# Performance work log

Measured on AMD Instinct MI355X. Metric: run time of the kernel, lower is better.

Reference implementation:

```python
import jax, jax.numpy as jnp
import numpy as np

B = 256      # graphs per batch
N = 512      # nodes per graph
FEAT = 64    # num_features
H = 64       # nhid
DEG = 16     # avg degree
RATIO = 0.5  # pooling_ratio
E = B * N * DEG


def setup_inputs() -> dict:
    key = jax.random.key(0)
    ks = jax.random.split(key, 12)
    # edges constructed within each graph via offsets
    src_loc = jax.random.randint(ks[0], (B, N * DEG), 0, N)
    dst_loc = jax.random.randint(ks[1], (B, N * DEG), 0, N)
    offs = (jnp.arange(B) * N)[:, None]
    edge_src = (src_loc + offs).reshape(-1).astype(jnp.int32)
    edge_dst = (dst_loc + offs).reshape(-1).astype(jnp.int32)
    batch = jnp.repeat(jnp.arange(B, dtype=jnp.int32), N)
    x = jax.random.normal(ks[2], (B * N, FEAT), dtype=jnp.float32)
    edge_attr = jax.random.uniform(ks[3], (E,), dtype=jnp.float32) + 0.1
    s1 = 1.0 / np.sqrt(FEAT)
    s2 = 1.0 / np.sqrt(H)
    return {
        "x": x,
        "edge_attr": edge_attr,
        "W1": jax.random.normal(ks[4], (FEAT, H), jnp.float32) * s1,
        "b1": jnp.zeros((H,), jnp.float32),
        "Wp1": jax.random.normal(ks[5], (H, 1), jnp.float32) * s2,
        "bp1": jnp.zeros((1,), jnp.float32),
        "W2": jax.random.normal(ks[6], (H, H), jnp.float32) * s2,
        "b2": jnp.zeros((H,), jnp.float32),
        "Wp2": jax.random.normal(ks[7], (H, 1), jnp.float32) * s2,
        "bp2": jnp.zeros((1,), jnp.float32),
        "edge_src": edge_src,
        "edge_dst": edge_dst,
        "batch": batch,
    }


def gcn_conv(x, W, b, src, dst, ew, n):
    """PyG GCNConv: sym-normalized weighted adjacency + self-loops (weight 1)."""
    h = x @ W                                   # [n, out]
    deg = jnp.zeros((n,), x.dtype).at[dst].add(ew) + 1.0  # self-loop adds 1
    dinv = jax.lax.rsqrt(deg)
    coef = dinv[dst] * ew * dinv[src]           # [E]
    out = jnp.zeros_like(h).at[dst].add(coef[:, None] * h[src])
    out = out + h * (1.0 / deg)[:, None]        # self-loop term: deg^-0.5 * 1 * deg^-0.5
    return out + b


def sag_pool(x, src, dst, ew, Wp, bp, n_per):
    """SAGPool: score = GCNConv(x)->1, per-graph top-k, gate by tanh(score),
    filter edges (dropped edges represented by zero weight)."""
    n = x.shape[0]
    score = gcn_conv(x, Wp, bp, src, dst, ew, n)[:, 0]   # [n]
    k = int(np.ceil(RATIO * n_per))
    _, idx = jax.lax.top_k(score.reshape(B, n_per), k)   # [B, k] local indices
    perm = (idx + (jnp.arange(B) * n_per)[:, None]).reshape(-1)
    xn = x[perm] * jnp.tanh(score[perm])[:, None]        # [B*k, H]
    newid = jnp.full((n,), -1, jnp.int32).at[perm].set(
        jnp.arange(B * k, dtype=jnp.int32))
    ns, nd = newid[src], newid[dst]
    valid = (ns >= 0) & (nd >= 0)
    ew2 = jnp.where(valid, ew, 0.0)
    ns = jnp.where(valid, ns, 0)
    nd = jnp.where(valid, nd, 0)
    return xn, ns, nd, ew2, k


def readout(x, k):
    """[gmp || gap] per graph; each graph has exactly k nodes, contiguous."""
    xg = x.reshape(B, k, -1)
    return jnp.concatenate([xg.max(axis=1), xg.mean(axis=1)], axis=1)  # [B, 2H]


def reference(x, edge_attr, W1, b1, Wp1, bp1, W2, b2, Wp2, bp2,
              edge_src, edge_dst, batch):
    n0 = x.shape[0]
    h = jax.nn.relu(gcn_conv(x, W1, b1, edge_src, edge_dst, edge_attr, n0))
    h, s1, d1, w1e, k1 = sag_pool(h, edge_src, edge_dst, edge_attr, Wp1, bp1, N)
    x1 = readout(h, k1)
    h = jax.nn.relu(gcn_conv(h, W2, b2, s1, d1, w1e, B * k1))
    h, _, _, _, k2 = sag_pool(h, s1, d1, w1e, Wp2, bp2, k1)
    x2 = readout(h, k2)
    return (x1 + x2) / 2.0
```

## Files before the change

kernel.cpp:

```cpp
#include <hip/hip_runtime.h>
#include <math.h>

#define BG   256
#define NN   512
#define EPG  (NN * 16)
#define NE   (BG * EPG)
#define N0   (BG * NN)
#define K1   256
#define N1_  (BG * K1)
#define K2   128
#define N2_  (BG * K2)

__device__ __forceinline__ float4 f4fma(float s, float4 a, float4 c) {
    c.x = fmaf(s, a.x, c.x); c.y = fmaf(s, a.y, c.y);
    c.z = fmaf(s, a.z, c.z); c.w = fmaf(s, a.w, c.w);
    return c;
}

template <int NPG, bool REMAP>
__global__ __launch_bounds__(512)
void stage_head_kernel(const int* __restrict__ esrc, const int* __restrict__ edst,
                       const float* __restrict__ eatt, const int* __restrict__ nid,
                       int2* __restrict__ pairs, int* __restrict__ rowstart,
                       int* __restrict__ rowcnt, float* __restrict__ dinv,
                       const float4* __restrict__ X4, const float4* __restrict__ W4,
                       float4* __restrict__ Y4, int nrows, int mmb) {
    __shared__ __align__(16) char smem[52224];
    if ((int)blockIdx.x < BG) {
        int2*  lpair = (int2*)smem;
        int*   cnt   = (int*)(smem + 32768);
        float* wsum  = (float*)(smem + 32768) + NPG;
        int*   scn   = (int*)(smem + 32768) + 2 * NPG;
        float* sdinv = (float*)(smem + 32768) + 3 * NPG;
        int*   wtot  = (int*)(smem + 32768) + 4 * NPG;
        int g = blockIdx.x;
        int e0 = g * EPG, nbase = g * NPG;
        for (int ii = threadIdx.x; ii < NPG; ii += 512) { cnt[ii] = 0; wsum[ii] = 0.f; }
        __syncthreads();
        const int4*   edst4 = (const int4*)(edst + e0);
        const int4*   esrc4 = (const int4*)(esrc + e0);
        const float4* eatt4 = (const float4*)(eatt + e0);
        int ed[16]; int es[16]; float ea[16];
#pragma unroll
        for (int c = 0; c < 4; ++c) {
            int ch = threadIdx.x + c * 512;
            int4   dd = edst4[ch];
            int4   ss = esrc4[ch];
            float4 ww = eatt4[ch];
            ed[c * 4 + 0] = dd.x; ed[c * 4 + 1] = dd.y; ed[c * 4 + 2] = dd.z; ed[c * 4 + 3] = dd.w;
            es[c * 4 + 0] = ss.x; es[c * 4 + 1] = ss.y; es[c * 4 + 2] = ss.z; es[c * 4 + 3] = ss.w;
            ea[c * 4 + 0] = ww.x; ea[c * 4 + 1] = ww.y; ea[c * 4 + 2] = ww.z; ea[c * 4 + 3] = ww.w;
        }
        if (REMAP) {
#pragma unroll
            for (int j = 0; j < 16; ++j) { ed[j] = nid[ed[j]]; es[j] = nid[es[j]]; }
        }
#pragma unroll
        for (int j = 0; j < 16; ++j) {
            bool valid = !REMAP || (ed[j] >= 0 && es[j] >= 0);
            if (valid) {
                int dl = ed[j] - nbase;
                atomicAdd(&cnt[dl], 1);
                atomicAdd(&wsum[dl], ea[j]);
            }
        }
        __syncthreads();
        int i = threadIdx.x;
        int lane = i & 63, wvid = i >> 6;
        int xval = (i < NPG) ? cnt[i] : 0;
        int xs = xval;
#pragma unroll
        for (int off = 1; off < 64; off <<= 1) {
            int v = __shfl_up(xs, off, 64);
            if (lane >= off) xs += v;
        }
        if (lane == 63) wtot[wvid] = xs;
        __syncthreads();
        int woff = 0, total = 0;
#pragma unroll
        for (int t = 0; t < 8; ++t) {
            int wt = wtot[t];
            if (t < wvid) woff += wt;
            total += wt;
        }
        xs += woff;
        if (i < NPG) {
            int st = xs - xval;
            rowstart[nbase + i] = e0 + st;
            rowcnt[nbase + i]   = xval;
            float di = rsqrtf(wsum[i] + 1.0f);
            dinv[nbase + i] = di;
            sdinv[i] = di;
            scn[i] = st;
        }
        __syncthreads();
        int slots[16]; float cf[16];
#pragma unroll
        for (int j = 0; j < 16; ++j) {
            bool valid = !REMAP || (ed[j] >= 0 && es[j] >= 0);
            slots[j] = -1;
            if (valid) {
                int dl = ed[j] - nbase, sl = es[j] - nbase;
                cf[j] = sdinv[dl] * ea[j] * sdinv[sl];
                slots[j] = atomicAdd(&scn[dl], 1);
            }
        }
#pragma unroll
        for (int j = 0; j < 16; ++j)
            if (slots[j] >= 0 && slots[j] < 4096)
                lpair[slots[j]] = make_int2(es[j] - nbase, __float_as_int(cf[j]));
        __syncthreads();
        int n0 = total < 4096 ? total : 4096;
        for (int k = threadIdx.x; k < n0; k += 512) pairs[e0 + k] = lpair[k];
        __syncthreads();
        if (total > 4096) {
#pragma unroll
            for (int j = 0; j < 16; ++j)
                if (slots[j] >= 4096)
                    lpair[slots[j] - 4096] = make_int2(es[j] - nbase, __float_as_int(cf[j]));
            __syncthreads();
            int n1 = total - 4096;
            for (int k = threadIdx.x; k < n1; k += 512) pairs[e0 + 4096 + k] = lpair[k];
        }
    } else {
        float (*sW)[68] = (float (*)[68])smem;
        int p = threadIdx.x >> 8;
        int t = threadIdx.x & 255;
        float (*sX)[68] = (float (*)[68])(smem + 17408 + p * 17408);
#pragma unroll
        for (int u = 0; u < 2; ++u) {
            int idx = threadIdx.x + u * 512;
            int r = idx >> 4, c4 = idx & 15;
            *(float4*)&sW[r][c4 * 4] = W4[idx];
        }
        int mb = blockIdx.x - BG;
        int ntiles = nrows >> 6;
        int rg = t >> 4, cg = t & 15;
        for (int tile = mb * 2 + p; tile < ntiles; tile += mmb * 2) {
            __syncthreads();
            int row0 = tile << 6;
#pragma unroll
            for (int u = 0; u < 4; ++u) {
                int idx = t + u * 256;
                int r = idx >> 4, c4 = idx & 15;
                *(float4*)&sX[r][c4 * 4] = X4[(size_t)(row0 + r) * 16 + c4];
            }
            __syncthreads();
            float4 acc0 = make_float4(0.f, 0.f, 0.f, 0.f);
            float4 acc1 = acc0, acc2 = acc0, acc3 = acc0;
#pragma unroll
            for (int k4 = 0; k4 < 16; ++k4) {
                float4 xv0 = *(const float4*)&sX[rg * 4 + 0][k4 * 4];
                float4 xv1 = *(const float4*)&sX[rg * 4 + 1][k4 * 4];
                float4 xv2 = *(const float4*)&sX[rg * 4 + 2][k4 * 4];
                float4 xv3 = *(const float4*)&sX[rg * 4 + 3][k4 * 4];
                float4 wv0 = *(const float4*)&sW[k4 * 4 + 0][cg * 4];
                float4 wv1 = *(const float4*)&sW[k4 * 4 + 1][cg * 4];
                float4 wv2 = *(const float4*)&sW[k4 * 4 + 2][cg * 4];
                float4 wv3 = *(const float4*)&sW[k4 * 4 + 3][cg * 4];
                acc0 = f4fma(xv0.x, wv0, acc0); acc0 = f4fma(xv0.y, wv1, acc0);
                acc0 = f4fma(xv0.z, wv2, acc0); acc0 = f4fma(xv0.w, wv3, acc0);
                acc1 = f4fma(xv1.x, wv0, acc1); acc1 = f4fma(xv1.y, wv1, acc1);
                acc1 = f4fma(xv1.z, wv2, acc1); acc1 = f4fma(xv1.w, wv3, acc1);
                acc2 = f4fma(xv2.x, wv0, acc2); acc2 = f4fma(xv2.y, wv1, acc2);
                acc2 = f4fma(xv2.z, wv2, acc2); acc2 = f4fma(xv2.w, wv3, acc2);
                acc3 = f4fma(xv3.x, wv0, acc3); acc3 = f4fma(xv3.y, wv1, acc3);
                acc3 = f4fma(xv3.z, wv2, acc3); acc3 = f4fma(xv3.w, wv3, acc3);
            }
            size_t ob = (size_t)(row0 + rg * 4) * 16 + cg;
            Y4[ob]      = acc0;
            Y4[ob + 16] = acc1;
            Y4[ob + 32] = acc2;
            Y4[ob + 48] = acc3;
        }
    }
}

template <int NPG, int K, bool FINAL>
__global__ __launch_bounds__(1024)
void tail_kernel(const float4* __restrict__ hx4, const int2* __restrict__ pairs,
                 const int* __restrict__ rowstart, const int* __restrict__ rowcnt,
                 const float* __restrict__ dinv, const float4* __restrict__ b4,
                 const float4* __restrict__ wp4, const float* __restrict__ bp,
                 int* __restrict__ nid, float4* __restrict__ xn4,
                 float* __restrict__ xr, const float* __restrict__ x1r,
                 float* __restrict__ out) {
    constexpr int PASSES = NPG / 32;
    constexpr int LPN = 1024 / NPG;
    constexpr int LOG_LPN = (LPN == 2) ? 1 : 2;
    constexpr int QF = 16 / LPN;
    constexpr int RLOG = (NPG == 512) ? 9 : 8;
    constexpr int RCH = NPG * NPG / 1024;
    constexpr int SH_A  = NPG * 68;
    constexpr int SH_UN = 4096;
    __shared__ __align__(16) float smem[SH_A + SH_UN + 2 * NPG + 64 + 64];
    float*  shx  = smem;
    int*    perm = (int*)(smem + SH_A);
    float*  shp  = smem + SH_A + NPG;
    float4* smx  = (float4*)(smem + SH_A);
    float4* ssm  = (float4*)(smem + SH_A + 2048);
    float*  ssc  = smem + SH_A + SH_UN;
    int*    rnk  = (int*)(smem + SH_A + SH_UN + NPG);
    float*  sbw  = smem + SH_A + SH_UN + 2 * NPG;
    int*    hist = (int*)(smem + SH_A + SH_UN + 2 * NPG + 64);

    int g = blockIdx.x, nbase = g * NPG;
    int t = threadIdx.x;
    int lane16 = t & 15, lane = t & 63;

    for (int i = t; i < NPG * 16; i += 1024) {
        int r = i >> 4, c4 = i & 15;
        *(float4*)&shx[r * 68 + c4 * 4] = hx4[(size_t)nbase * 16 + i];
    }
    if (t < 64) { sbw[t] = ((const float*)b4)[t]; hist[t] = 0; }
    for (int i = t; i < NPG; i += 1024) rnk[i] = 0;
    __syncthreads();
    for (int i = t; i < NPG; i += 1024) {
        int c = min(rowcnt[nbase + i], 63);
        atomicAdd(&hist[c], 1);
    }
    __syncthreads();
    if (t < 64) {
        int v = hist[t], s = v;
#pragma unroll
        for (int off = 1; off < 64; off <<= 1) {
            int u = __shfl_up(s, off, 64);
            if (lane >= off) s += u;
        }
        hist[t] = s - v;
    }
    __syncthreads();
    for (int i = t; i < NPG; i += 1024) {
        int c = min(rowcnt[nbase + i], 63);
        int pos = atomicAdd(&hist[c], 1);
        perm[pos] = i;
    }
    __syncthreads();
    {
        int idx2 = t >> LOG_LPN;
        int half = t & (LPN - 1);
        int nl = perm[idx2];
        int st = rowstart[nbase + nl], cn = rowcnt[nbase + nl];
        float di = dinv[nbase + nl], dii = di * di;
        int fb = half * QF;
        float4 acc[QF];
#pragma unroll
        for (int c = 0; c < QF; ++c) {
            float4 xv = *(const float4*)&shx[nl * 68 + (fb + c) * 4];
            acc[c].x = fmaf(xv.x, dii, sbw[(fb + c) * 4 + 0]);
            acc[c].y = fmaf(xv.y, dii, sbw[(fb + c) * 4 + 1]);
            acc[c].z = fmaf(xv.z, dii, sbw[(fb + c) * 4 + 2]);
            acc[c].w = fmaf(xv.w, dii, sbw[(fb + c) * 4 + 3]);
        }
        int2 p0 = (cn > 0) ? pairs[st] : make_int2(0, 0);
        int2 p1 = (cn > 1) ? pairs[st + 1] : make_int2(0, 0);
        for (int j = 0; j < cn; ++j) {
            int2 p2 = (j + 2 < cn) ? pairs[st + j + 2] : make_int2(0, 0);
            float cf = __int_as_float(p0.y);
            int   s  = p0.x;
#pragma unroll
            for (int c = 0; c < QF; ++c)
                acc[c] = f4fma(cf, *(const float4*)&shx[s * 68 + (fb + c) * 4], acc[c]);
            p0 = p1; p1 = p2;
        }
#pragma unroll
        for (int c = 0; c < QF; ++c) {
            acc[c].x = fmaxf(acc[c].x, 0.f); acc[c].y = fmaxf(acc[c].y, 0.f);
            acc[c].z = fmaxf(acc[c].z, 0.f); acc[c].w = fmaxf(acc[c].w, 0.f);
        }
        __syncthreads();
#pragma unroll
        for (int c = 0; c < QF; ++c)
            *(float4*)&shx[nl * 68 + (fb + c) * 4] = acc[c];
    }
    __syncthreads();
    if (t < 512) {
        int wv8 = t >> 6, sub4 = (t >> 4) & 3;
        float4 w4 = wp4[lane16];
#pragma unroll
        for (int p = 0; p < PASSES; ++p) {
            int n2 = p * 32 + wv8 * 4 + sub4;
            float4 a = *(const float4*)&shx[n2 * 68 + lane16 * 4];
            float tt = a.x * w4.x + a.y * w4.y + a.z * w4.z + a.w * w4.w;
            tt += __shfl_xor(tt, 1, 64); tt += __shfl_xor(tt, 2, 64);
            tt += __shfl_xor(tt, 4, 64); tt += __shfl_xor(tt, 8, 64);
            if (lane16 == 0) shp[n2] = tt;
        }
    }
    __syncthreads();
    if (t < NPG) {
        int i = perm[t];
        int st = rowstart[nbase + i], cn = rowcnt[nbase + i];
        float di = dinv[nbase + i];
        float a = fmaf(shp[i], di * di, bp[0]);
        int2 q0 = (cn > 0) ? pairs[st] : make_int2(0, 0);
        int2 q1 = (cn > 1) ? pairs[st + 1] : make_int2(0, 0);
        for (int j = 0; j < cn; ++j) {
            int2 q2 = (j + 2 < cn) ? pairs[st + j + 2] : make_int2(0, 0);
            a = fmaf(__int_as_float(q0.y), shp[q0.x], a);
            q0 = q1; q1 = q2;
        }
        ssc[i] = a;
    }
    __syncthreads();
    {
        int part = t >> RLOG;
        int i = t & (NPG - 1);
        float si = ssc[i];
        int j0 = part * RCH;
        int rank = 0;
        for (int j = j0; j < j0 + RCH; j += 4) {
            float4 sj = *(const float4*)&ssc[j];
            rank += (sj.x > si) || (sj.x == si && j     < i);
            rank += (sj.y > si) || (sj.y == si && j + 1 < i);
            rank += (sj.z > si) || (sj.z == si && j + 2 < i);
            rank += (sj.w > si) || (sj.w == si && j + 3 < i);
        }
        atomicAdd(&rnk[i], rank);
    }
    __syncthreads();
    if (!FINAL)
        for (int i = t; i < NPG; i += 1024)
            nid[nbase + i] = (rnk[i] < K) ? (g * K + rnk[i]) : -1;
    float4 mx = make_float4(-3.402823466e38f, -3.402823466e38f, -3.402823466e38f, -3.402823466e38f);
    float4 sm = make_float4(0.f, 0.f, 0.f, 0.f);
    if (t < 512) {
        int wv8 = t >> 6, sub4 = (t >> 4) & 3;
#pragma unroll
        for (int p = 0; p < PASSES; ++p) {
            int n2 = p * 32 + wv8 * 4 + sub4;
            int r = rnk[n2];
            if (r < K) {
                float gt = tanhf(ssc[n2]);
                float4 v = *(const float4*)&shx[n2 * 68 + lane16 * 4];
                v.x *= gt; v.y *= gt; v.z *= gt; v.w *= gt;
                if (!FINAL) xn4[((size_t)g * K + r) * 16 + lane16] = v;
                mx.x = fmaxf(mx.x, v.x); mx.y = fmaxf(mx.y, v.y);
                mx.z = fmaxf(mx.z, v.z); mx.w = fmaxf(mx.w, v.w);
                sm.x += v.x; sm.y += v.y; sm.z += v.z; sm.w += v.w;
            }
        }
    }
    int grp = t >> 4;
    __syncthreads();
    if (t < 512) {
        smx[grp * 16 + lane16] = mx;
        ssm[grp * 16 + lane16] = sm;
    }
    __syncthreads();
    if (grp == 0) {
#pragma unroll
        for (int u = 1; u < 32; ++u) {
            float4 a = smx[u * 16 + lane16], b = ssm[u * 16 + lane16];
            mx.x = fmaxf(mx.x, a.x); mx.y = fmaxf(mx.y, a.y);
            mx.z = fmaxf(mx.z, a.z); mx.w = fmaxf(mx.w, a.w);
            sm.x += b.x; sm.y += b.y; sm.z += b.z; sm.w += b.w;
        }
        float invK = 1.f / K;
        int c = lane16 * 4;
        float mr[4] = {mx.x, mx.y, mx.z, mx.w};
        float ar[4] = {sm.x * invK, sm.y * invK, sm.z * invK, sm.w * invK};
#pragma unroll
        for (int u = 0; u < 4; ++u) {
            if (FINAL) {
                out[g * 128 + c + u]      = 0.5f * (x1r[g * 128 + c + u]      + mr[u]);
                out[g * 128 + 64 + c + u] = 0.5f * (x1r[g * 128 + 64 + c + u] + ar[u]);
            } else {
                xr[g * 128 + c + u]      = mr[u];
                xr[g * 128 + 64 + c + u] = ar[u];
            }
        }
    }
}

extern "C" void kernel_launch(void* const* d_in, const int* in_sizes, int n_in,
                              void* d_out, int out_size, void* d_ws, size_t ws_size,
                              hipStream_t stream) {
    const float* x    = (const float*)d_in[0];
    const float* eatt = (const float*)d_in[1];
    const float* W1   = (const float*)d_in[2];
    const float* b1   = (const float*)d_in[3];
    const float* Wp1  = (const float*)d_in[4];
    const float* bp1  = (const float*)d_in[5];
    const float* W2   = (const float*)d_in[6];
    const float* b2   = (const float*)d_in[7];
    const float* Wp2  = (const float*)d_in[8];
    const float* bp2  = (const float*)d_in[9];
    const int*   esrc = (const int*)d_in[10];
    const int*   edst = (const int*)d_in[11];
    float* out = (float*)d_out;

    float* ws = (float*)d_ws;
    size_t o = 0;
    float* A    = ws + o; o += (size_t)N0 * 64;
    float* xn1  = ws + o; o += (size_t)N1_ * 64;
    int2*  prs  = (int2*)(ws + o); o += (size_t)NE * 2;
    int*   rst  = (int*)(ws + o); o += N0;
    int*   rcn  = (int*)(ws + o); o += N0;
    float* dinv = ws + o; o += N0;
    int*   nid  = (int*)(ws + o); o += N0;
    float* x1r  = ws + o; o += BG * 128;

    float* hx1 = A;
    float* hx2 = A;

    stage_head_kernel<NN, false><<<BG + 512, 512, 0, stream>>>(
        esrc, edst, eatt, nullptr, prs, rst, rcn, dinv,
        (const float4*)x, (const float4*)W1, (float4*)hx1, N0, 512);
    tail_kernel<NN, K1, false><<<BG, 1024, 0, stream>>>(
        (const float4*)hx1, prs, rst, rcn, dinv, (const float4*)b1,
        (const float4*)Wp1, bp1, nid, (float4*)xn1, x1r, nullptr, nullptr);
    stage_head_kernel<K1, true><<<BG + 256, 512, 0, stream>>>(
        esrc, edst, eatt, nid, prs, rst, rcn, dinv,
        (const float4*)xn1, (const float4*)W2, (float4*)hx2, N1_, 256);
    tail_kernel<K1, K2, true><<<BG, 1024, 0, stream>>>(
        (const float4*)hx2, prs, rst, rcn, dinv, (const float4*)b2,
        (const float4*)Wp2, bp2, nullptr, nullptr, nullptr, x1r, out);
}
```

Baseline: 218.1 us.

## Fuse CSR build, feature matmul and tail into one per-graph stage kernel

Merges the head kernel (edge bucketing into CSR plus a separate matmul block range) with the tail kernel into a single per-graph kernel of 1024 threads. The matmul now runs from the node features already staged in shared memory and writes the result back into that buffer, so the intermediate feature matrix no longer round-trips through global memory and two launches are removed. The cost is that each stage now launches only 256 blocks, one per graph, so the matmul and edge work are serialized inside each block instead of overlapping across extra blocks, and register pressure rises from holding the accumulated tiles.

```diff
diff --git a/kernel.cpp b/kernel.cpp
--- a/kernel.cpp
+++ b/kernel.cpp
@@ -17,174 +17,18 @@
     return c;
 }
 
-template <int NPG, bool REMAP>
-__global__ __launch_bounds__(512)
-void stage_head_kernel(const int* __restrict__ esrc, const int* __restrict__ edst,
-                       const float* __restrict__ eatt, const int* __restrict__ nid,
-                       int2* __restrict__ pairs, int* __restrict__ rowstart,
-                       int* __restrict__ rowcnt, float* __restrict__ dinv,
-                       const float4* __restrict__ X4, const float4* __restrict__ W4,
-                       float4* __restrict__ Y4, int nrows, int mmb) {
-    __shared__ __align__(16) char smem[52224];
-    if ((int)blockIdx.x < BG) {
-        int2*  lpair = (int2*)smem;
-        int*   cnt   = (int*)(smem + 32768);
-        float* wsum  = (float*)(smem + 32768) + NPG;
-        int*   scn   = (int*)(smem + 32768) + 2 * NPG;
-        float* sdinv = (float*)(smem + 32768) + 3 * NPG;
-        int*   wtot  = (int*)(smem + 32768) + 4 * NPG;
-        int g = blockIdx.x;
-        int e0 = g * EPG, nbase = g * NPG;
-        for (int ii = threadIdx.x; ii < NPG; ii += 512) { cnt[ii] = 0; wsum[ii] = 0.f; }
-        __syncthreads();
-        const int4*   edst4 = (const int4*)(edst + e0);
-        const int4*   esrc4 = (const int4*)(esrc + e0);
-        const float4* eatt4 = (const float4*)(eatt + e0);
-        int ed[16]; int es[16]; float ea[16];
-#pragma unroll
-        for (int c = 0; c < 4; ++c) {
-            int ch = threadIdx.x + c * 512;
-            int4   dd = edst4[ch];
-            int4   ss = esrc4[ch];
-            float4 ww = eatt4[ch];
-            ed[c * 4 + 0] = dd.x; ed[c * 4 + 1] = dd.y; ed[c * 4 + 2] = dd.z; ed[c * 4 + 3] = dd.w;
-            es[c * 4 + 0] = ss.x; es[c * 4 + 1] = ss.y; es[c * 4 + 2] = ss.z; es[c * 4 + 3] = ss.w;
-            ea[c * 4 + 0] = ww.x; ea[c * 4 + 1] = ww.y; ea[c * 4 + 2] = ww.z; ea[c * 4 + 3] = ww.w;
-        }
-        if (REMAP) {
-#pragma unroll
-            for (int j = 0; j < 16; ++j) { ed[j] = nid[ed[j]]; es[j] = nid[es[j]]; }
-        }
-#pragma unroll
-        for (int j = 0; j < 16; ++j) {
-            bool valid = !REMAP || (ed[j] >= 0 && es[j] >= 0);
-            if (valid) {
-                int dl = ed[j] - nbase;
-                atomicAdd(&cnt[dl], 1);
-                atomicAdd(&wsum[dl], ea[j]);
-            }
-        }
-        __syncthreads();
-        int i = threadIdx.x;
-        int lane = i & 63, wvid = i >> 6;
-        int xval = (i < NPG) ? cnt[i] : 0;
-        int xs = xval;
-#pragma unroll
-        for (int off = 1; off < 64; off <<= 1) {
-            int v = __shfl_up(xs, off, 64);
-            if (lane >= off) xs += v;
-        }
-        if (lane == 63) wtot[wvid] = xs;
-        __syncthreads();
-        int woff = 0, total = 0;
-#pragma unroll
-        for (int t = 0; t < 8; ++t) {
-            int wt = wtot[t];
-            if (t < wvid) woff += wt;
-            total += wt;
-        }
-        xs += woff;
-        if (i < NPG) {
-            int st = xs - xval;
-            rowstart[nbase + i] = e0 + st;
-            rowcnt[nbase + i]   = xval;
-            float di = rsqrtf(wsum[i] + 1.0f);
-            dinv[nbase + i] = di;
-            sdinv[i] = di;
-            scn[i] = st;
-        }
-        __syncthreads();
-        int slots[16]; float cf[16];
-#pragma unroll
-        for (int j = 0; j < 16; ++j) {
-            bool valid = !REMAP || (ed[j] >= 0 && es[j] >= 0);
-            slots[j] = -1;
-            if (valid) {
-                int dl = ed[j] - nbase, sl = es[j] - nbase;
-                cf[j] = sdinv[dl] * ea[j] * sdinv[sl];
-                slots[j] = atomicAdd(&scn[dl], 1);
-            }
-        }
-#pragma unroll
-        for (int j = 0; j < 16; ++j)
-            if (slots[j] >= 0 && slots[j] < 4096)
-                lpair[slots[j]] = make_int2(es[j] - nbase, __float_as_int(cf[j]));
-        __syncthreads();
-        int n0 = total < 4096 ? total : 4096;
-        for (int k = threadIdx.x; k < n0; k += 512) pairs[e0 + k] = lpair[k];
-        __syncthreads();
-        if (total > 4096) {
-#pragma unroll
-            for (int j = 0; j < 16; ++j)
-                if (slots[j] >= 4096)
-                    lpair[slots[j] - 4096] = make_int2(es[j] - nbase, __float_as_int(cf[j]));
-            __syncthreads();
-            int n1 = total - 4096;
-            for (int k = threadIdx.x; k < n1; k += 512) pairs[e0 + 4096 + k] = lpair[k];
-        }
-    } else {
-        float (*sW)[68] = (float (*)[68])smem;
-        int p = threadIdx.x >> 8;
-        int t = threadIdx.x & 255;
-        float (*sX)[68] = (float (*)[68])(smem + 17408 + p * 17408);
-#pragma unroll
-        for (int u = 0; u < 2; ++u) {
-            int idx = threadIdx.x + u * 512;
-            int r = idx >> 4, c4 = idx & 15;
-            *(float4*)&sW[r][c4 * 4] = W4[idx];
-        }
-        int mb = blockIdx.x - BG;
-        int ntiles = nrows >> 6;
-        int rg = t >> 4, cg = t & 15;
-        for (int tile = mb * 2 + p; tile < ntiles; tile += mmb * 2) {
-            __syncthreads();
-            int row0 = tile << 6;
-#pragma unroll
-            for (int u = 0; u < 4; ++u) {
-                int idx = t + u * 256;
-                int r = idx >> 4, c4 = idx & 15;
-                *(float4*)&sX[r][c4 * 4] = X4[(size_t)(row0 + r) * 16 + c4];
-            }
-            __syncthreads();
-            float4 acc0 = make_float4(0.f, 0.f, 0.f, 0.f);
-            float4 acc1 = acc0, acc2 = acc0, acc3 = acc0;
-#pragma unroll
-            for (int k4 = 0; k4 < 16; ++k4) {
-                float4 xv0 = *(const float4*)&sX[rg * 4 + 0][k4 * 4];
-                float4 xv1 = *(const float4*)&sX[rg * 4 + 1][k4 * 4];
-                float4 xv2 = *(const float4*)&sX[rg * 4 + 2][k4 * 4];
-                float4 xv3 = *(const float4*)&sX[rg * 4 + 3][k4 * 4];
-                float4 wv0 = *(const float4*)&sW[k4 * 4 + 0][cg * 4];
-                float4 wv1 = *(const float4*)&sW[k4 * 4 + 1][cg * 4];
-                float4 wv2 = *(const float4*)&sW[k4 * 4 + 2][cg * 4];
-                float4 wv3 = *(const float4*)&sW[k4 * 4 + 3][cg * 4];
-                acc0 = f4fma(xv0.x, wv0, acc0); acc0 = f4fma(xv0.y, wv1, acc0);
-                acc0 = f4fma(xv0.z, wv2, acc0); acc0 = f4fma(xv0.w, wv3, acc0);
-                acc1 = f4fma(xv1.x, wv0, acc1); acc1 = f4fma(xv1.y, wv1, acc1);
-                acc1 = f4fma(xv1.z, wv2, acc1); acc1 = f4fma(xv1.w, wv3, acc1);
-                acc2 = f4fma(xv2.x, wv0, acc2); acc2 = f4fma(xv2.y, wv1, acc2);
-                acc2 = f4fma(xv2.z, wv2, acc2); acc2 = f4fma(xv2.w, wv3, acc2);
-                acc3 = f4fma(xv3.x, wv0, acc3); acc3 = f4fma(xv3.y, wv1, acc3);
-                acc3 = f4fma(xv3.z, wv2, acc3); acc3 = f4fma(xv3.w, wv3, acc3);
-            }
-            size_t ob = (size_t)(row0 + rg * 4) * 16 + cg;
-            Y4[ob]      = acc0;
-            Y4[ob + 16] = acc1;
-            Y4[ob + 32] = acc2;
-            Y4[ob + 48] = acc3;
-        }
-    }
-}
-
-template <int NPG, int K, bool FINAL>
+template <int NPG, int K, bool REMAP, bool FINAL>
 __global__ __launch_bounds__(1024)
-void tail_kernel(const float4* __restrict__ hx4, const int2* __restrict__ pairs,
-                 const int* __restrict__ rowstart, const int* __restrict__ rowcnt,
-                 const float* __restrict__ dinv, const float4* __restrict__ b4,
-                 const float4* __restrict__ wp4, const float* __restrict__ bp,
-                 int* __restrict__ nid, float4* __restrict__ xn4,
-                 float* __restrict__ xr, const float* __restrict__ x1r,
-                 float* __restrict__ out) {
+void stage_kernel(const int* __restrict__ esrc, const int* __restrict__ edst,
+                  const float* __restrict__ eatt, const int* __restrict__ nid_in,
+                  int* __restrict__ nid_out,
+                  int2* __restrict__ pairs, int* __restrict__ rowstart,
+                  int* __restrict__ rowcnt, float* __restrict__ dinv,
+                  const float4* __restrict__ X4, const float4* __restrict__ W4,
+                  const float4* __restrict__ b4, const float4* __restrict__ wp4,
+                  const float* __restrict__ bp,
+                  float4* __restrict__ xn4, float* __restrict__ xr,
+                  const float* __restrict__ x1r, float* __restrict__ out) {
     constexpr int PASSES = NPG / 32;
     constexpr int LPN = 1024 / NPG;
     constexpr int LOG_LPN = (LPN == 2) ? 1 : 2;
@@ -203,18 +47,164 @@
     int*    rnk  = (int*)(smem + SH_A + SH_UN + NPG);
     float*  sbw  = smem + SH_A + SH_UN + 2 * NPG;
     int*    hist = (int*)(smem + SH_A + SH_UN + 2 * NPG + 64);
-
-    int g = blockIdx.x, nbase = g * NPG;
+    int2*   lpair = (int2*)smem;
+    int*    cnt   = (int*)smem + 8192;
+    float*  wsum  = smem + 8192 + NPG;
+    int*    scn   = (int*)smem + 8192 + 2 * NPG;
+    float*  sdinv = smem + 8192 + 3 * NPG;
+    int*    wtot  = (int*)smem + 8192 + 4 * NPG;
+    float*  sWf   = smem + SH_A;
+
+    int g = blockIdx.x, nbase = g * NPG, e0 = g * EPG;
     int t = threadIdx.x;
     int lane16 = t & 15, lane = t & 63;
 
+    for (int i = t; i < NPG; i += 1024) { cnt[i] = 0; wsum[i] = 0.f; }
+    __syncthreads();
+    {
+        const int4*   edst4 = (const int4*)(edst + e0);
+        const int4*   esrc4 = (const int4*)(esrc + e0);
+        const float4* eatt4 = (const float4*)(eatt + e0);
+        int ed[8]; int es[8]; float ea[8];
+#pragma unroll
+        for (int c = 0; c < 2; ++c) {
+            int ch = t + c * 1024;
+            int4   dd = edst4[ch];
+            int4   ss = esrc4[ch];
+            float4 ww = eatt4[ch];
+            ed[c * 4 + 0] = dd.x; ed[c * 4 + 1] = dd.y; ed[c * 4 + 2] = dd.z; ed[c * 4 + 3] = dd.w;
+            es[c * 4 + 0] = ss.x; es[c * 4 + 1] = ss.y; es[c * 4 + 2] = ss.z; es[c * 4 + 3] = ss.w;
+            ea[c * 4 + 0] = ww.x; ea[c * 4 + 1] = ww.y; ea[c * 4 + 2] = ww.z; ea[c * 4 + 3] = ww.w;
+        }
+        if (REMAP) {
+#pragma unroll
+            for (int j = 0; j < 8; ++j) { ed[j] = nid_in[ed[j]]; es[j] = nid_in[es[j]]; }
+        }
+#pragma unroll
+        for (int j = 0; j < 8; ++j) {
+            bool valid = !REMAP || (ed[j] >= 0 && es[j] >= 0);
+            if (valid) {
+                int dl = ed[j] - nbase;
+                atomicAdd(&cnt[dl], 1);
+                atomicAdd(&wsum[dl], ea[j]);
+            }
+        }
+        __syncthreads();
+        int wv = t >> 6;
+        int xval = (t < NPG) ? cnt[t] : 0;
+        int xs = xval;
+#pragma unroll
+        for (int off = 1; off < 64; off <<= 1) {
+            int v = __shfl_up(xs, off, 64);
+            if (lane >= off) xs += v;
+        }
+        if (lane == 63) wtot[wv] = xs;
+        __syncthreads();
+        int woff = 0, total = 0;
+#pragma unroll
+        for (int w = 0; w < 16; ++w) {
+            int wt = wtot[w];
+            if (w < wv) woff += wt;
+            total += wt;
+        }
+        xs += woff;
+        if (t < NPG) {
+            int st = xs - xval;
+            rowstart[nbase + t] = e0 + st;
+            rowcnt[nbase + t]   = xval;
+            float di = rsqrtf(wsum[t] + 1.0f);
+            dinv[nbase + t] = di;
+            sdinv[t] = di;
+            scn[t] = st;
+        }
+        __syncthreads();
+        int slots[8]; float cf[8];
+#pragma unroll
+        for (int j = 0; j < 8; ++j) {
+            bool valid = !REMAP || (ed[j] >= 0 && es[j] >= 0);
+            slots[j] = -1;
+            if (valid) {
+                int dl = ed[j] - nbase, sl = es[j] - nbase;
+                cf[j] = sdinv[dl] * ea[j] * sdinv[sl];
+                slots[j] = atomicAdd(&scn[dl], 1);
+            }
+        }
+#pragma unroll
+        for (int j = 0; j < 8; ++j)
+            if (slots[j] >= 0 && slots[j] < 4096)
+                lpair[slots[j]] = make_int2(es[j] - nbase, __float_as_int(cf[j]));
+        __syncthreads();
+        int n0 = total < 4096 ? total : 4096;
+        for (int k2 = t; k2 < n0; k2 += 1024) pairs[e0 + k2] = lpair[k2];
+        __syncthreads();
+        if (total > 4096) {
+#pragma unroll
+            for (int j = 0; j < 8; ++j)
+                if (slots[j] >= 4096)
+                    lpair[slots[j] - 4096] = make_int2(es[j] - nbase, __float_as_int(cf[j]));
+            __syncthreads();
+            int n1 = total - 4096;
+            for (int k2 = t; k2 < n1; k2 += 1024) pairs[e0 + 4096 + k2] = lpair[k2];
+            __syncthreads();
+        }
+    }
+    __syncthreads();
+
     for (int i = t; i < NPG * 16; i += 1024) {
         int r = i >> 4, c4 = i & 15;
-        *(float4*)&shx[r * 68 + c4 * 4] = hx4[(size_t)nbase * 16 + i];
+        *(float4*)&shx[r * 68 + c4 * 4] = X4[(size_t)nbase * 16 + i];
+    }
+    {
+        int r = t >> 4, c4 = t & 15;
+        *(float4*)&sWf[r * 68 + c4 * 4] = W4[t];
+    }
+    __syncthreads();
+
+    {
+        constexpr int TILES = NPG / 64, TPG = TILES / 4;
+        int q = t >> 8, tq = t & 255;
+        int rg = tq >> 4, cg = tq & 15;
+        float4 ac[TPG][4];
+#pragma unroll
+        for (int tt = 0; tt < TPG; ++tt) {
+            int row0 = (tt * 4 + q) * 64;
+            float4 acc0 = make_float4(0.f, 0.f, 0.f, 0.f);
+            float4 acc1 = acc0, acc2 = acc0, acc3 = acc0;
+#pragma unroll
+            for (int k4 = 0; k4 < 16; ++k4) {
+                float4 xv0 = *(const float4*)&shx[(row0 + rg * 4 + 0) * 68 + k4 * 4];
+                float4 xv1 = *(const float4*)&shx[(row0 + rg * 4 + 1) * 68 + k4 * 4];
+                float4 xv2 = *(const float4*)&shx[(row0 + rg * 4 + 2) * 68 + k4 * 4];
+                float4 xv3 = *(const float4*)&shx[(row0 + rg * 4 + 3) * 68 + k4 * 4];
+                float4 wv0 = *(const float4*)&sWf[(k4 * 4 + 0) * 68 + cg * 4];
+                float4 wv1 = *(const float4*)&sWf[(k4 * 4 + 1) * 68 + cg * 4];
+                float4 wv2 = *(const float4*)&sWf[(k4 * 4 + 2) * 68 + cg * 4];
+                float4 wv3 = *(const float4*)&sWf[(k4 * 4 + 3) * 68 + cg * 4];
+                acc0 = f4fma(xv0.x, wv0, acc0); acc0 = f4fma(xv0.y, wv1, acc0);
+                acc0 = f4fma(xv0.z, wv2, acc0); acc0 = f4fma(xv0.w, wv3, acc0);
+                acc1 = f4fma(xv1.x, wv0, acc1); acc1 = f4fma(xv1.y, wv1, acc1);
+                acc1 = f4fma(xv1.z, wv2, acc1); acc1 = f4fma(xv1.w, wv3, acc1);
+                acc2 = f4fma(xv2.x, wv0, acc2); acc2 = f4fma(xv2.y, wv1, acc2);
+                acc2 = f4fma(xv2.z, wv2, acc2); acc2 = f4fma(xv2.w, wv3, acc2);
+                acc3 = f4fma(xv3.x, wv0, acc3); acc3 = f4fma(xv3.y, wv1, acc3);
+                acc3 = f4fma(xv3.z, wv2, acc3); acc3 = f4fma(xv3.w, wv3, acc3);
+            }
+            ac[tt][0] = acc0; ac[tt][1] = acc1; ac[tt][2] = acc2; ac[tt][3] = acc3;
+        }
+        __syncthreads();
+#pragma unroll
+        for (int tt = 0; tt < TPG; ++tt) {
+            int row0 = (tt * 4 + q) * 64;
+            *(float4*)&shx[(row0 + rg * 4 + 0) * 68 + cg * 4] = ac[tt][0];
+            *(float4*)&shx[(row0 + rg * 4 + 1) * 68 + cg * 4] = ac[tt][1];
+            *(float4*)&shx[(row0 + rg * 4 + 2) * 68 + cg * 4] = ac[tt][2];
+            *(float4*)&shx[(row0 + rg * 4 + 3) * 68 + cg * 4] = ac[tt][3];
+        }
     }
     if (t < 64) { sbw[t] = ((const float*)b4)[t]; hist[t] = 0; }
     for (int i = t; i < NPG; i += 1024) rnk[i] = 0;
     __syncthreads();
+
     for (int i = t; i < NPG; i += 1024) {
         int c = min(rowcnt[nbase + i], 63);
         atomicAdd(&hist[c], 1);
@@ -256,11 +246,11 @@
         int2 p1 = (cn > 1) ? pairs[st + 1] : make_int2(0, 0);
         for (int j = 0; j < cn; ++j) {
             int2 p2 = (j + 2 < cn) ? pairs[st + j + 2] : make_int2(0, 0);
-            float cf = __int_as_float(p0.y);
-            int   s  = p0.x;
+            float cfv = __int_as_float(p0.y);
+            int   s   = p0.x;
 #pragma unroll
             for (int c = 0; c < QF; ++c)
-                acc[c] = f4fma(cf, *(const float4*)&shx[s * 68 + (fb + c) * 4], acc[c]);
+                acc[c] = f4fma(cfv, *(const float4*)&shx[s * 68 + (fb + c) * 4], acc[c]);
             p0 = p1; p1 = p2;
         }
 #pragma unroll
@@ -321,7 +311,7 @@
     __syncthreads();
     if (!FINAL)
         for (int i = t; i < NPG; i += 1024)
-            nid[nbase + i] = (rnk[i] < K) ? (g * K + rnk[i]) : -1;
+            nid_out[nbase + i] = (rnk[i] < K) ? (g * K + rnk[i]) : -1;
     float4 mx = make_float4(-3.402823466e38f, -3.402823466e38f, -3.402823466e38f, -3.402823466e38f);
     float4 sm = make_float4(0.f, 0.f, 0.f, 0.f);
     if (t < 512) {
@@ -400,20 +390,14 @@
     float* dinv = ws + o; o += N0;
     int*   nid  = (int*)(ws + o); o += N0;
     float* x1r  = ws + o; o += BG * 128;
-
-    float* hx1 = A;
-    float* hx2 = A;
-
-    stage_head_kernel<NN, false><<<BG + 512, 512, 0, stream>>>(
-        esrc, edst, eatt, nullptr, prs, rst, rcn, dinv,
-        (const float4*)x, (const float4*)W1, (float4*)hx1, N0, 512);
-    tail_kernel<NN, K1, false><<<BG, 1024, 0, stream>>>(
-        (const float4*)hx1, prs, rst, rcn, dinv, (const float4*)b1,
-        (const float4*)Wp1, bp1, nid, (float4*)xn1, x1r, nullptr, nullptr);
-    stage_head_kernel<K1, true><<<BG + 256, 512, 0, stream>>>(
-        esrc, edst, eatt, nid, prs, rst, rcn, dinv,
-        (const float4*)xn1, (const float4*)W2, (float4*)hx2, N1_, 256);
-    tail_kernel<K1, K2, true><<<BG, 1024, 0, stream>>>(
-        (const float4*)hx2, prs, rst, rcn, dinv, (const float4*)b2,
-        (const float4*)Wp2, bp2, nullptr, nullptr, nullptr, x1r, out);
+    (void)A;
+
+    stage_kernel<NN, K1, false, false><<<BG, 1024, 0, stream>>>(
+        esrc, edst, eatt, nullptr, nid, prs, rst, rcn, dinv,
+        (const float4*)x, (const float4*)W1, (const float4*)b1,
+        (const float4*)Wp1, bp1, (float4*)xn1, x1r, nullptr, nullptr);
+    stage_kernel<K1, K2, true, true><<<BG, 1024, 0, stream>>>(
+        esrc, edst, eatt, nid, nullptr, prs, rst, rcn, dinv,
+        (const float4*)xn1, (const float4*)W2, (const float4*)b2,
+        (const float4*)Wp2, bp2, nullptr, nullptr, x1r, out);
 }
```

New measurement: 207.2 us. 5.0% less time.
